# Kernel tuning notes

Hardware: AMD Instinct MI355X
Metric: run time of the kernel (lower is better)

The kernel has to match this reference:

```python
import math
import jax, jax.numpy as jnp
import numpy as np

CAPACITY_FACTOR = 1.0
MIN_CAPACITY = 8


def setup_inputs() -> dict:
    key = jax.random.key(0)
    k1, k2 = jax.random.split(key)
    s, d, e = 8192, 1024, 64
    inputs = jax.random.normal(k1, (s, d), dtype=jnp.float32)
    wg_weight = jax.random.normal(k2, (e, d), dtype=jnp.float32) * (1.0 / math.sqrt(d))
    return {"inputs": inputs, "wg_weight": wg_weight}


def reference(inputs, wg_weight):
    # gate projection (always fp32 in the original)
    logits = inputs.astype(jnp.float32) @ wg_weight.T  # [s, e]
    s, e = logits.shape
    # static capacity: ceil(s/e * capacity_factor), floored at min_capacity
    capacity = max(int(math.ceil(s / e * CAPACITY_FACTOR)), MIN_CAPACITY)

    gates = jax.nn.softmax(logits, axis=1)            # [s, e]
    indices = jnp.argmax(gates, axis=1)               # [s]
    mask = jax.nn.one_hot(indices, e, dtype=jnp.int32)  # [s, e]
    exp_counts = jnp.sum(mask, axis=0)                # [e]

    # load-balancing aux loss (uses mask BEFORE capacity dropping)
    me = jnp.mean(gates, axis=0)
    ce = jnp.mean(mask.astype(jnp.float32), axis=0)
    l_aux = jnp.sum(me * ce) * e

    # capacity dropping: with use_rts=False, topk over the binary mask keeps
    # the first `capacity` tokens routed to each expert, i.e. cumulative
    # position-in-expert < capacity
    positions = jnp.cumsum(mask, axis=0) - 1          # [s, e]
    mask = mask * (positions < capacity).astype(jnp.int32)

    locations = jnp.cumsum(mask, axis=0) - 1          # [s, e]
    locations_s = jnp.sum(locations * mask, axis=1)   # [s] slot per token

    gates = gates * mask.astype(jnp.float32)          # zero out dropped tokens
    locations_sc = jax.nn.one_hot(locations_s, capacity, dtype=jnp.float32)  # [s, c]
    combine_weights = jnp.einsum('se,sc->sec', gates, locations_sc)  # [s, e, c]
    dispatch_mask = combine_weights.astype(bool)
    return l_aux, combine_weights, dispatch_mask, exp_counts
```

## Files before the change

### kernel.cpp

```cpp
#include <hip/hip_runtime.h>
#include <cstdint>
#include <cstddef>

#define S 8192
#define Dm 1024
#define E 64
#define CAP 128
#define SEC 67108864ull

#define GEMM_BLOCKS 256
#define SCAN_BLOCKS 64
#define FILL_BLOCKS 1984
#define N4F 33554432u
#define WSCALE 4096.0f
#define INV_WSCALE (1.0f / 4096.0f)

typedef float f32x4 __attribute__((ext_vector_type(4)));
typedef _Float16 f16x4 __attribute__((ext_vector_type(4)));
typedef _Float16 f16x8 __attribute__((ext_vector_type(8)));

#define CV4(H, L, ROW, COL, V, SCALE) do {                                     \
    f16x4 hh, ll; float t_;                                                    \
    t_ = (V).x * (SCALE); hh[0] = (_Float16)t_; ll[0] = (_Float16)(t_ - (float)hh[0]); \
    t_ = (V).y * (SCALE); hh[1] = (_Float16)t_; ll[1] = (_Float16)(t_ - (float)hh[1]); \
    t_ = (V).z * (SCALE); hh[2] = (_Float16)t_; ll[2] = (_Float16)(t_ - (float)hh[2]); \
    t_ = (V).w * (SCALE); hh[3] = (_Float16)t_; ll[3] = (_Float16)(t_ - (float)hh[3]); \
    *(f16x4*)&H[ROW][COL] = hh;                                                \
    *(f16x4*)&L[ROW][COL] = ll;                                                \
} while (0)

__global__ __launch_bounds__(512) void k_gemm(const float* __restrict__ x,
                                              const float* __restrict__ w,
                                              float* __restrict__ gate,
                                              int* __restrict__ idx,
                                              float* __restrict__ me_part) {
    int bid = blockIdx.x;
    int tid = threadIdx.x;
    __shared__ _Float16 Ah[32][72];
    __shared__ _Float16 Alo[32][72];
    __shared__ _Float16 Wh[64][72];
    __shared__ _Float16 Wlo[64][72];
    __shared__ float Sl[32][66];
    __shared__ float sm[32];
    __shared__ float sinv[32];
    int t0 = bid * 32;
    int ar = tid >> 4;
    int ac = (tid & 15) * 4;
    int wr = tid >> 3;
    int wc = (tid & 7) * 8;
    const float* asrc = x + (size_t)(t0 + ar) * Dm + ac;
    const float* wsrc = w + (size_t)wr * Dm + wc;

    int wv = tid >> 6;
    int l = tid & 63;
    int lr = l & 15;
    int lg = l >> 4;
    int mt = wv & 1;
    int nt = wv >> 1;
    f32x4 acc = {0.f, 0.f, 0.f, 0.f};

    float4 pa = *(const float4*)(asrc + 0);
    float4 pw0 = *(const float4*)(wsrc + 0);
    float4 pw1 = *(const float4*)(wsrc + 4);
    float4 qa = *(const float4*)(asrc + 64);
    float4 qw0 = *(const float4*)(wsrc + 64);
    float4 qw1 = *(const float4*)(wsrc + 68);

#define WRITE_LDS(A, W0, W1)                                                   \
    CV4(Ah, Alo, ar, ac, A, 1.0f);                                             \
    CV4(Wh, Wlo, wr, wc, W0, WSCALE);                                          \
    CV4(Wh, Wlo, wr, (wc + 4), W1, WSCALE);

#define LOADP(KB)                                                              \
    pa = *(const float4*)(asrc + (KB));                                        \
    pw0 = *(const float4*)(wsrc + (KB));                                       \
    pw1 = *(const float4*)(wsrc + (KB) + 4);

#define LOADQ(KB)                                                              \
    qa = *(const float4*)(asrc + (KB));                                        \
    qw0 = *(const float4*)(wsrc + (KB));                                       \
    qw1 = *(const float4*)(wsrc + (KB) + 4);

#define INNER_MFMA                                                             \
    _Pragma("unroll")                                                          \
    for (int ks = 0; ks < 2; ++ks) {                                           \
        int kc = ks * 32 + lg * 8;                                             \
        f16x8 ah = *(const f16x8*)&Ah[mt * 16 + lr][kc];                       \
        f16x8 al = *(const f16x8*)&Alo[mt * 16 + lr][kc];                      \
        f16x8 bh = *(const f16x8*)&Wh[nt * 16 + lr][kc];                       \
        f16x8 bl = *(const f16x8*)&Wlo[nt * 16 + lr][kc];                      \
        acc = __builtin_amdgcn_mfma_f32_16x16x32_f16(ah, bh, acc, 0, 0, 0);    \
        acc = __builtin_amdgcn_mfma_f32_16x16x32_f16(al, bh, acc, 0, 0, 0);    \
        acc = __builtin_amdgcn_mfma_f32_16x16x32_f16(ah, bl, acc, 0, 0, 0);    \
    }

    for (int ch = 0; ch < 16; ch += 2) {
        __syncthreads();
        WRITE_LDS(pa, pw0, pw1)
        __syncthreads();
        if (ch + 2 < 16) { LOADP((ch + 2) * 64) }
        INNER_MFMA
        __syncthreads();
        WRITE_LDS(qa, qw0, qw1)
        __syncthreads();
        if (ch + 3 < 16) { LOADQ((ch + 3) * 64) }
        INNER_MFMA
    }
#undef WRITE_LDS
#undef LOADP
#undef LOADQ
#undef INNER_MFMA
    __syncthreads();
#pragma unroll
    for (int r = 0; r < 4; ++r)
        Sl[mt * 16 + lg * 4 + r][nt * 16 + lr] = acc[r] * INV_WSCALE;
    __syncthreads();
    if (tid < 32) {
        float m = Sl[tid][0];
        int am = 0;
#pragma unroll
        for (int c = 1; c < E; ++c) {
            float v = Sl[tid][c];
            if (v > m) { m = v; am = c; }
        }
        float ssum = 0.f;
#pragma unroll
        for (int c = 0; c < E; ++c) ssum += __expf(Sl[tid][c] - m);
        float inv = 1.0f / ssum;
        gate[t0 + tid] = inv;
        idx[t0 + tid] = am;
        sm[tid] = m;
        sinv[tid] = inv;
    }
    __syncthreads();
    if (tid < E) {
        float cs = 0.f;
#pragma unroll 8
        for (int r = 0; r < 32; ++r)
            cs += __expf(Sl[r][tid] - sm[r]) * sinv[r];
        me_part[bid * E + tid] = cs;
    }
}

__global__ __launch_bounds__(256) void k_fillscan(const int* __restrict__ idx,
                                                  const float* __restrict__ gate,
                                                  const float* __restrict__ me_part,
                                                  float2* __restrict__ tg,
                                                  float* __restrict__ la_part,
                                                  float* __restrict__ out) {
    int bid = blockIdx.x;
    int tid = threadIdx.x;
    if (bid < SCAN_BLOCKS) {
        __shared__ int wsum[4];
        __shared__ float red[256];
        int e = bid;
        int lane = tid & 63;
        int wid = tid >> 6;
        if (bid == 0 && tid == 0) {
            out[1] = 0.f; out[2] = 0.f; out[3] = 0.f;
            out[2 * SEC] = 0.f;
        }
        int running = 0;
        for (int ch = 0; ch < S / 256; ++ch) {
            int t = ch * 256 + tid;
            bool f = (idx[t] == e);
            unsigned long long b = __ballot(f);
            int pre = __popcll(b & ((1ull << lane) - 1ull));
            if (lane == 0) wsum[wid] = __popcll(b);
            __syncthreads();
            int off = running;
#pragma unroll
            for (int w2 = 0; w2 < 4; ++w2)
                if (w2 < wid) off += wsum[w2];
            int p = off + pre;
            if (f) {
                int tgt = (p < CAP) ? e * CAP + p : -1;
                tg[t] = make_float2(__int_as_float(tgt), gate[t]);
            }
            running += wsum[0] + wsum[1] + wsum[2] + wsum[3];
            __syncthreads();
        }
        red[tid] = me_part[tid * E + e];
        __syncthreads();
        for (int s2 = 128; s2 > 0; s2 >>= 1) {
            if (tid < s2) red[tid] += red[tid + s2];
            __syncthreads();
        }
        if (tid == 0) {
            out[1 + 2 * SEC + e] = (float)running;
            la_part[e] = red[0] * (1.0f / (float)S) *
                         ((float)running / (float)S) * (float)E;
        }
    } else {
        int fb = bid - SCAN_BLOCKS;
        f32x4 z = {0.f, 0.f, 0.f, 0.f};
        f32x4* o4 = (f32x4*)out;
        for (unsigned i = 1u + (unsigned)fb * 256u + tid; i < N4F;
             i += FILL_BLOCKS * 256u)
            o4[i] = z;
    }
}

__global__ __launch_bounds__(256) void k_scatter(const float2* __restrict__ tg,
                                                 const float* __restrict__ la_part,
                                                 float* __restrict__ out) {
    int bid = blockIdx.x;
    int tid = threadIdx.x;
    if (bid == 32) {
        if (tid < E) {
            float la = la_part[tid];
#pragma unroll
            for (int off = 32; off > 0; off >>= 1)
                la += __shfl_down(la, off, 64);
            if (tid == 0) out[0] = la;
        }
        return;
    }
    int t = bid * 256 + tid;
    float2 g = tg[t];
    int tgt = __float_as_int(g.x);
    if (tgt >= 0) {
        size_t o = 1 + (size_t)t * (E * CAP) + (size_t)tgt;
        out[o] = g.y;
        out[o + SEC] = 1.0f;
    }
}

extern "C" void kernel_launch(void* const* d_in, const int* in_sizes, int n_in,
                              void* d_out, int out_size, void* d_ws, size_t ws_size,
                              hipStream_t stream) {
    const float* x = (const float*)d_in[0];
    const float* w = (const float*)d_in[1];
    float* out = (float*)d_out;

    float* me_part = (float*)d_ws;
    float* gate = me_part + GEMM_BLOCKS * E;
    int* idx = (int*)(gate + S);
    float2* tg = (float2*)(idx + S);
    float* la_part = (float*)(tg + S);

    k_gemm<<<dim3(GEMM_BLOCKS), dim3(512), 0, stream>>>(x, w, gate, idx, me_part);
    k_fillscan<<<dim3(SCAN_BLOCKS + FILL_BLOCKS), dim3(256), 0, stream>>>(
        idx, gate, me_part, tg, la_part, out);
    k_scatter<<<dim3(33), dim3(256), 0, stream>>>(tg, la_part, out);
}
```

Before: 150.4 us.

## Overlap dispatch-mask zero fill with gate GEMM and fuse combine zeroing into scatter

The zero fill of the dispatch-mask half of the output now runs in extra blocks of the GEMM kernel, so it overlaps the gate projection. The combine-weights half is written densely by a merge kernel, where each block writes full rows with the gate value at the routed slot. This replaces the separate zero-then-scatter pass. The per-expert scan is split into four quarters per expert, seeded by per-block expert counts computed in the GEMM epilogue, which gives it more parallelism. The aux loss is reduced with an atomicAdd. The cost is an extra count buffer, a larger grid for the first kernel, and reliance on exact index arithmetic for the split fill ranges.

Measured after the change: 128.9 us, median of 2. 14.3% less time.

```diff
diff --git a/kernel.cpp b/kernel.cpp
--- a/kernel.cpp
+++ b/kernel.cpp
@@ -9,9 +9,11 @@
 #define SEC 67108864ull
 
 #define GEMM_BLOCKS 256
-#define SCAN_BLOCKS 64
-#define FILL_BLOCKS 1984
-#define N4F 33554432u
+#define FILL_BLOCKS 1792
+#define B0 16777217u
+#define TCH 16777231u
+#define CH 9363u
+#define N4END 33554448u
 #define WSCALE 4096.0f
 #define INV_WSCALE (1.0f / 4096.0f)
 
@@ -29,200 +31,229 @@
     *(f16x4*)&L[ROW][COL] = ll;                                                \
 } while (0)
 
-__global__ __launch_bounds__(512) void k_gemm(const float* __restrict__ x,
+__global__ __launch_bounds__(512) void k_main(const float* __restrict__ x,
                                               const float* __restrict__ w,
                                               float* __restrict__ gate,
                                               int* __restrict__ idx,
-                                              float* __restrict__ me_part) {
+                                              float* __restrict__ me_part,
+                                              int* __restrict__ cnt_g,
+                                              float* __restrict__ la_ws,
+                                              float* __restrict__ out) {
     int bid = blockIdx.x;
     int tid = threadIdx.x;
-    __shared__ _Float16 Ah[32][72];
-    __shared__ _Float16 Alo[32][72];
-    __shared__ _Float16 Wh[64][72];
-    __shared__ _Float16 Wlo[64][72];
-    __shared__ float Sl[32][66];
-    __shared__ float sm[32];
-    __shared__ float sinv[32];
-    int t0 = bid * 32;
-    int ar = tid >> 4;
-    int ac = (tid & 15) * 4;
-    int wr = tid >> 3;
-    int wc = (tid & 7) * 8;
-    const float* asrc = x + (size_t)(t0 + ar) * Dm + ac;
-    const float* wsrc = w + (size_t)wr * Dm + wc;
-
-    int wv = tid >> 6;
-    int l = tid & 63;
-    int lr = l & 15;
-    int lg = l >> 4;
-    int mt = wv & 1;
-    int nt = wv >> 1;
-    f32x4 acc = {0.f, 0.f, 0.f, 0.f};
-
-    float4 pa = *(const float4*)(asrc + 0);
-    float4 pw0 = *(const float4*)(wsrc + 0);
-    float4 pw1 = *(const float4*)(wsrc + 4);
-    float4 qa = *(const float4*)(asrc + 64);
-    float4 qw0 = *(const float4*)(wsrc + 64);
-    float4 qw1 = *(const float4*)(wsrc + 68);
+    if (bid < GEMM_BLOCKS) {
+        __shared__ _Float16 Ah[32][72];
+        __shared__ _Float16 Alo[32][72];
+        __shared__ _Float16 Wh[64][72];
+        __shared__ _Float16 Wlo[64][72];
+        __shared__ float Sl[32][66];
+        __shared__ float sm[32];
+        __shared__ float sinv[32];
+        __shared__ int sidx[32];
+        int t0 = bid * 32;
+        int ar = tid >> 4;
+        int ac = (tid & 15) * 4;
+        int wr = tid >> 3;
+        int wc = (tid & 7) * 8;
+        const float* asrc = x + (size_t)(t0 + ar) * Dm + ac;
+        const float* wsrc = w + (size_t)wr * Dm + wc;
+
+        int wv = tid >> 6;
+        int l = tid & 63;
+        int lr = l & 15;
+        int lg = l >> 4;
+        int mt = wv & 1;
+        int nt = wv >> 1;
+        f32x4 acc = {0.f, 0.f, 0.f, 0.f};
+
+        float4 pa = *(const float4*)(asrc + 0);
+        float4 pw0 = *(const float4*)(wsrc + 0);
+        float4 pw1 = *(const float4*)(wsrc + 4);
+        float4 qa = *(const float4*)(asrc + 64);
+        float4 qw0 = *(const float4*)(wsrc + 64);
+        float4 qw1 = *(const float4*)(wsrc + 68);
 
 #define WRITE_LDS(A, W0, W1)                                                   \
-    CV4(Ah, Alo, ar, ac, A, 1.0f);                                             \
-    CV4(Wh, Wlo, wr, wc, W0, WSCALE);                                          \
-    CV4(Wh, Wlo, wr, (wc + 4), W1, WSCALE);
-
+        CV4(Ah, Alo, ar, ac, A, 1.0f);                                         \
+        CV4(Wh, Wlo, wr, wc, W0, WSCALE);                                      \
+        CV4(Wh, Wlo, wr, (wc + 4), W1, WSCALE);
 #define LOADP(KB)                                                              \
-    pa = *(const float4*)(asrc + (KB));                                        \
-    pw0 = *(const float4*)(wsrc + (KB));                                       \
-    pw1 = *(const float4*)(wsrc + (KB) + 4);
-
+        pa = *(const float4*)(asrc + (KB));                                    \
+        pw0 = *(const float4*)(wsrc + (KB));                                   \
+        pw1 = *(const float4*)(wsrc + (KB) + 4);
 #define LOADQ(KB)                                                              \
-    qa = *(const float4*)(asrc + (KB));                                        \
-    qw0 = *(const float4*)(wsrc + (KB));                                       \
-    qw1 = *(const float4*)(wsrc + (KB) + 4);
-
+        qa = *(const float4*)(asrc + (KB));                                    \
+        qw0 = *(const float4*)(wsrc + (KB));                                   \
+        qw1 = *(const float4*)(wsrc + (KB) + 4);
 #define INNER_MFMA                                                             \
-    _Pragma("unroll")                                                          \
-    for (int ks = 0; ks < 2; ++ks) {                                           \
-        int kc = ks * 32 + lg * 8;                                             \
-        f16x8 ah = *(const f16x8*)&Ah[mt * 16 + lr][kc];                       \
-        f16x8 al = *(const f16x8*)&Alo[mt * 16 + lr][kc];                      \
-        f16x8 bh = *(const f16x8*)&Wh[nt * 16 + lr][kc];                       \
-        f16x8 bl = *(const f16x8*)&Wlo[nt * 16 + lr][kc];                      \
-        acc = __builtin_amdgcn_mfma_f32_16x16x32_f16(ah, bh, acc, 0, 0, 0);    \
-        acc = __builtin_amdgcn_mfma_f32_16x16x32_f16(al, bh, acc, 0, 0, 0);    \
-        acc = __builtin_amdgcn_mfma_f32_16x16x32_f16(ah, bl, acc, 0, 0, 0);    \
-    }
-
-    for (int ch = 0; ch < 16; ch += 2) {
-        __syncthreads();
-        WRITE_LDS(pa, pw0, pw1)
-        __syncthreads();
-        if (ch + 2 < 16) { LOADP((ch + 2) * 64) }
-        INNER_MFMA
-        __syncthreads();
-        WRITE_LDS(qa, qw0, qw1)
-        __syncthreads();
-        if (ch + 3 < 16) { LOADQ((ch + 3) * 64) }
-        INNER_MFMA
-    }
+        _Pragma("unroll")                                                      \
+        for (int ks = 0; ks < 2; ++ks) {                                       \
+            int kc = ks * 32 + lg * 8;                                         \
+            f16x8 ah = *(const f16x8*)&Ah[mt * 16 + lr][kc];                   \
+            f16x8 al = *(const f16x8*)&Alo[mt * 16 + lr][kc];                  \
+            f16x8 bh = *(const f16x8*)&Wh[nt * 16 + lr][kc];                   \
+            f16x8 bl = *(const f16x8*)&Wlo[nt * 16 + lr][kc];                  \
+            acc = __builtin_amdgcn_mfma_f32_16x16x32_f16(ah, bh, acc, 0, 0, 0); \
+            acc = __builtin_amdgcn_mfma_f32_16x16x32_f16(al, bh, acc, 0, 0, 0); \
+            acc = __builtin_amdgcn_mfma_f32_16x16x32_f16(ah, bl, acc, 0, 0, 0); \
+        }
+
+        for (int ch = 0; ch < 16; ch += 2) {
+            __syncthreads();
+            WRITE_LDS(pa, pw0, pw1)
+            __syncthreads();
+            if (ch + 2 < 16) { LOADP((ch + 2) * 64) }
+            INNER_MFMA
+            __syncthreads();
+            WRITE_LDS(qa, qw0, qw1)
+            __syncthreads();
+            if (ch + 3 < 16) { LOADQ((ch + 3) * 64) }
+            INNER_MFMA
+        }
 #undef WRITE_LDS
 #undef LOADP
 #undef LOADQ
 #undef INNER_MFMA
+        __syncthreads();
+#pragma unroll
+        for (int r = 0; r < 4; ++r)
+            Sl[mt * 16 + lg * 4 + r][nt * 16 + lr] = acc[r] * INV_WSCALE;
+        __syncthreads();
+        if (tid < 32) {
+            float m = Sl[tid][0];
+            int am = 0;
+#pragma unroll
+            for (int c = 1; c < E; ++c) {
+                float v = Sl[tid][c];
+                if (v > m) { m = v; am = c; }
+            }
+            float ssum = 0.f;
+#pragma unroll
+            for (int c = 0; c < E; ++c) ssum += __expf(Sl[tid][c] - m);
+            float inv = 1.0f / ssum;
+            gate[t0 + tid] = inv;
+            idx[t0 + tid] = am;
+            sm[tid] = m;
+            sinv[tid] = inv;
+            sidx[tid] = am;
+        }
+        __syncthreads();
+        if (tid < E) {
+            float cs = 0.f;
+            int cnt = 0;
+#pragma unroll 8
+            for (int r = 0; r < 32; ++r) {
+                cs += __expf(Sl[r][tid] - sm[r]) * sinv[r];
+                cnt += (sidx[r] == tid) ? 1 : 0;
+            }
+            me_part[bid * E + tid] = cs;
+            cnt_g[bid * E + tid] = cnt;
+        }
+    } else {
+        int fb = bid - GEMM_BLOCKS;
+        if (fb == 0 && tid == 0) {
+            out[1 + SEC] = 0.f; out[2 + SEC] = 0.f; out[3 + SEC] = 0.f;
+            la_ws[0] = 0.f;
+        }
+        unsigned base = B0 + (unsigned)fb * CH;
+        f32x4 z = {0.f, 0.f, 0.f, 0.f};
+        f32x4* o4 = (f32x4*)out;
+        for (unsigned j = tid; j < CH; j += 512u) {
+            unsigned i = base + j;
+            if (i < N4END) o4[i] = z;
+        }
+    }
+}
+
+__global__ __launch_bounds__(256) void k_scan(const int* __restrict__ idx,
+                                              const float* __restrict__ gate,
+                                              const float* __restrict__ me_part,
+                                              const int* __restrict__ cnt_g,
+                                              float2* __restrict__ tg,
+                                              float* __restrict__ la_ws,
+                                              float* __restrict__ out) {
+    int e = blockIdx.x >> 2;
+    int q = blockIdx.x & 3;
+    int tid = threadIdx.x;
+    int lane = tid & 63;
+    int wid = tid >> 6;
+    __shared__ int wsum[4];
+    __shared__ int ired[256];
+    __shared__ float red[256];
+    int nb = q << 6;
+    int a = 0;
+    for (int b = tid; b < nb; b += 256) a += cnt_g[b * E + e];
+    ired[tid] = a;
     __syncthreads();
-#pragma unroll
-    for (int r = 0; r < 4; ++r)
-        Sl[mt * 16 + lg * 4 + r][nt * 16 + lr] = acc[r] * INV_WSCALE;
+    for (int s2 = 128; s2 > 0; s2 >>= 1) {
+        if (tid < s2) ired[tid] += ired[tid + s2];
+        __syncthreads();
+    }
+    int running = ired[0];
     __syncthreads();
-    if (tid < 32) {
-        float m = Sl[tid][0];
-        int am = 0;
-#pragma unroll
-        for (int c = 1; c < E; ++c) {
-            float v = Sl[tid][c];
-            if (v > m) { m = v; am = c; }
-        }
-        float ssum = 0.f;
-#pragma unroll
-        for (int c = 0; c < E; ++c) ssum += __expf(Sl[tid][c] - m);
-        float inv = 1.0f / ssum;
-        gate[t0 + tid] = inv;
-        idx[t0 + tid] = am;
-        sm[tid] = m;
-        sinv[tid] = inv;
-    }
-    __syncthreads();
-    if (tid < E) {
-        float cs = 0.f;
-#pragma unroll 8
-        for (int r = 0; r < 32; ++r)
-            cs += __expf(Sl[r][tid] - sm[r]) * sinv[r];
-        me_part[bid * E + tid] = cs;
-    }
-}
-
-__global__ __launch_bounds__(256) void k_fillscan(const int* __restrict__ idx,
-                                                  const float* __restrict__ gate,
-                                                  const float* __restrict__ me_part,
-                                                  float2* __restrict__ tg,
-                                                  float* __restrict__ la_part,
-                                                  float* __restrict__ out) {
+    for (int ch = 0; ch < 8; ++ch) {
+        int t = q * 2048 + ch * 256 + tid;
+        bool f = (idx[t] == e);
+        unsigned long long b = __ballot(f);
+        int pre = __popcll(b & ((1ull << lane) - 1ull));
+        if (lane == 0) wsum[wid] = __popcll(b);
+        __syncthreads();
+        int off = running;
+#pragma unroll
+        for (int w2 = 0; w2 < 4; ++w2)
+            if (w2 < wid) off += wsum[w2];
+        int p = off + pre;
+        if (f) {
+            int tgt = (p < CAP) ? e * CAP + p : -1;
+            tg[t] = make_float2(__int_as_float(tgt), gate[t]);
+        }
+        running += wsum[0] + wsum[1] + wsum[2] + wsum[3];
+        __syncthreads();
+    }
+    if (q == 3) {
+        red[tid] = me_part[tid * E + e];
+        __syncthreads();
+        for (int s2 = 128; s2 > 0; s2 >>= 1) {
+            if (tid < s2) red[tid] += red[tid + s2];
+            __syncthreads();
+        }
+        if (tid == 0) {
+            out[1 + 2 * (size_t)SEC + e] = (float)running;
+            float la = red[0] * (1.0f / (float)S) *
+                       ((float)running / (float)S) * (float)E;
+            atomicAdd(la_ws, la);
+        }
+    }
+}
+
+__global__ __launch_bounds__(256) void k_merge(const float2* __restrict__ tg,
+                                               const float* __restrict__ la_ws,
+                                               float* __restrict__ out) {
     int bid = blockIdx.x;
     int tid = threadIdx.x;
-    if (bid < SCAN_BLOCKS) {
-        __shared__ int wsum[4];
-        __shared__ float red[256];
-        int e = bid;
-        int lane = tid & 63;
-        int wid = tid >> 6;
-        if (bid == 0 && tid == 0) {
-            out[1] = 0.f; out[2] = 0.f; out[3] = 0.f;
-            out[2 * SEC] = 0.f;
-        }
-        int running = 0;
-        for (int ch = 0; ch < S / 256; ++ch) {
-            int t = ch * 256 + tid;
-            bool f = (idx[t] == e);
-            unsigned long long b = __ballot(f);
-            int pre = __popcll(b & ((1ull << lane) - 1ull));
-            if (lane == 0) wsum[wid] = __popcll(b);
-            __syncthreads();
-            int off = running;
-#pragma unroll
-            for (int w2 = 0; w2 < 4; ++w2)
-                if (w2 < wid) off += wsum[w2];
-            int p = off + pre;
-            if (f) {
-                int tgt = (p < CAP) ? e * CAP + p : -1;
-                tg[t] = make_float2(__int_as_float(tgt), gate[t]);
-            }
-            running += wsum[0] + wsum[1] + wsum[2] + wsum[3];
-            __syncthreads();
-        }
-        red[tid] = me_part[tid * E + e];
-        __syncthreads();
-        for (int s2 = 128; s2 > 0; s2 >>= 1) {
-            if (tid < s2) red[tid] += red[tid + s2];
-            __syncthreads();
-        }
-        if (tid == 0) {
-            out[1 + 2 * SEC + e] = (float)running;
-            la_part[e] = red[0] * (1.0f / (float)S) *
-                         ((float)running / (float)S) * (float)E;
-        }
-    } else {
-        int fb = bid - SCAN_BLOCKS;
-        f32x4 z = {0.f, 0.f, 0.f, 0.f};
-        f32x4* o4 = (f32x4*)out;
-        for (unsigned i = 1u + (unsigned)fb * 256u + tid; i < N4F;
-             i += FILL_BLOCKS * 256u)
-            o4[i] = z;
-    }
-}
-
-__global__ __launch_bounds__(256) void k_scatter(const float2* __restrict__ tg,
-                                                 const float* __restrict__ la_part,
-                                                 float* __restrict__ out) {
-    int bid = blockIdx.x;
-    int tid = threadIdx.x;
-    if (bid == 32) {
-        if (tid < E) {
-            float la = la_part[tid];
-#pragma unroll
-            for (int off = 32; off > 0; off >>= 1)
-                la += __shfl_down(la, off, 64);
-            if (tid == 0) out[0] = la;
-        }
-        return;
-    }
-    int t = bid * 256 + tid;
-    float2 g = tg[t];
-    int tgt = __float_as_int(g.x);
-    if (tgt >= 0) {
-        size_t o = 1 + (size_t)t * (E * CAP) + (size_t)tgt;
-        out[o] = g.y;
-        out[o + SEC] = 1.0f;
+    if (bid == 0 && tid == 0) out[0] = la_ws[0];
+    f32x4* o4 = (f32x4*)out;
+#pragma unroll
+    for (int k = 0; k < 4; ++k) {
+        int t = bid * 4 + k;
+        float2 g = tg[t];
+        int tgt = __float_as_int(g.x);
+        float gv = g.y;
+        for (int j = 1 + tid; j < 2048; j += 256) {
+            int base = 4 * j - 1;
+            f32x4 v;
+            v[0] = (tgt == base) ? gv : 0.f;
+            v[1] = (tgt == base + 1) ? gv : 0.f;
+            v[2] = (tgt == base + 2) ? gv : 0.f;
+            v[3] = (tgt == base + 3) ? gv : 0.f;
+            o4[2048u * (unsigned)t + (unsigned)j] = v;
+        }
+        if (tid < 4) {
+            int c = (tid < 3) ? tid : 8191;
+            out[1 + (size_t)t * 8192 + c] = (tgt == c) ? gv : 0.f;
+        }
+        if (tid == 4 && tgt >= 0)
+            out[1 + SEC + (size_t)t * 8192 + tgt] = 1.0f;
     }
 }
 
@@ -236,11 +267,13 @@
     float* me_part = (float*)d_ws;
     float* gate = me_part + GEMM_BLOCKS * E;
     int* idx = (int*)(gate + S);
-    float2* tg = (float2*)(idx + S);
-    float* la_part = (float*)(tg + S);
-
-    k_gemm<<<dim3(GEMM_BLOCKS), dim3(512), 0, stream>>>(x, w, gate, idx, me_part);
-    k_fillscan<<<dim3(SCAN_BLOCKS + FILL_BLOCKS), dim3(256), 0, stream>>>(
-        idx, gate, me_part, tg, la_part, out);
-    k_scatter<<<dim3(33), dim3(256), 0, stream>>>(tg, la_part, out);
-}
+    int* cnt_g = idx + S;
+    float2* tg = (float2*)(cnt_g + GEMM_BLOCKS * E);
+    float* la_ws = (float*)(tg + S);
+
+    k_main<<<dim3(GEMM_BLOCKS + FILL_BLOCKS), dim3(512), 0, stream>>>(
+        x, w, gate, idx, me_part, cnt_g, la_ws, out);
+    k_scan<<<dim3(256), dim3(256), 0, stream>>>(
+        idx, gate, me_part, cnt_g, tg, la_ws, out);
+    k_merge<<<dim3(2048), dim3(256), 0, stream>>>(tg, la_ws, out);
+}
```
